# Performance work log

Measured on AMD Instinct MI355X. Metric: run time of the kernel, lower is better.

The kernel has to match this reference:

```python
import jax, jax.numpy as jnp
import numpy as np

R = 16
LORA_ALPHA = 16
SCALING = LORA_ALPHA / R  # 1.0


def setup_inputs() -> dict:
    key = jax.random.key(0)
    kx, kr, ka = jax.random.split(key, 3)
    B, S, D, DO, E = 4, 2048, 4096, 4096, 8
    x = jax.random.normal(kx, (B, S, D), dtype=jnp.float32)
    # kaiming_uniform_(a=sqrt(5)) on Linear weight of fan_in=D -> U(-1/sqrt(D), 1/sqrt(D))
    bound_r = 1.0 / np.sqrt(D)
    route_w = jax.random.uniform(kr, (E, D), jnp.float32, -bound_r, bound_r)  # lora_route.weight
    bound_a = 1.0 / np.sqrt(D)
    A = jax.random.uniform(ka, (E, R, D), jnp.float32, -bound_a, bound_a)  # stacked lora_A{i}.weight [r, D]
    # lora_B weights are zero-initialized in the module; use small random for a nontrivial baseline
    kb = jax.random.fold_in(key, 7)
    Bw = jax.random.normal(kb, (E, DO, R), dtype=jnp.float32) * 0.02  # stacked lora_B{i}.weight [DO, r]
    return {"x": x, "route_w": route_w, "A": A, "Bw": Bw}


def reference(x, route_w, A, Bw):
    # router logits [B, S, E]
    logits = jnp.einsum("bsd,ed->bse", x, route_w)
    # top-1 hard routing: keep raw logit value at the argmax slot, zero elsewhere
    topk_v, topk_idx = jax.lax.top_k(logits, 1)  # [B,S,1]
    E = logits.shape[-1]
    route_weight = jax.nn.one_hot(topk_idx[..., 0], E, dtype=logits.dtype) * topk_v  # [B,S,E]
    # low-rank per-expert projections (dense over experts, as in the original loop)
    h = jnp.einsum("bsd,erd->bser", x, A)            # [B,S,E,r]
    wh = route_weight[..., None] * h                  # weight before the up-projection
    out = jnp.einsum("bser,eor->bso", wh, Bw) * SCALING  # [B,S,DO]
    return out
```

## Files before the change

kernel.cpp:

```cpp
#include <hip/hip_runtime.h>
#include <hip/hip_bf16.h>

#define DD   4096
#define NE   8
#define NR   16
#define NTOK 8192
#define NDO  4096
#define TAU  0.01f
#define MAXFLAG 8000

typedef __attribute__((ext_vector_type(8))) __bf16 bf16x8;
typedef __attribute__((ext_vector_type(4))) __bf16 bf16x4;
typedef __attribute__((ext_vector_type(4))) float  f32x4;

__device__ __forceinline__ bf16x8 to_bf16x8(float4 a, float4 b) {
    bf16x8 r;
    r[0] = (__bf16)a.x; r[1] = (__bf16)a.y; r[2] = (__bf16)a.z; r[3] = (__bf16)a.w;
    r[4] = (__bf16)b.x; r[5] = (__bf16)b.y; r[6] = (__bf16)b.z; r[7] = (__bf16)b.w;
    return r;
}

__device__ __forceinline__ bf16x8 zero_frag() {
    bf16x8 z;
    #pragma unroll
    for (int j = 0; j < 8; j++) z[j] = (__bf16)0.0f;
    return z;
}

__global__ __launch_bounds__(256) void k_prep_w(const float* __restrict__ rw,
                                                const float* __restrict__ Am,
                                                const float* __restrict__ Bw,
                                                __bf16* __restrict__ rwhl,
                                                __bf16* __restrict__ Ab,
                                                __bf16* __restrict__ Bwb) {
    const int b = blockIdx.x;
    if (b < 1024) {
        const int o = (b & 511) * 1024 + threadIdx.x * 4;
        const float4 v = *(const float4*)(((b < 512) ? Bw : Am) + o);
        bf16x4 p;
        p[0] = (__bf16)v.x; p[1] = (__bf16)v.y; p[2] = (__bf16)v.z; p[3] = (__bf16)v.w;
        *(bf16x4*)(((b < 512) ? Bwb : Ab) + o) = p;
    } else {
        const int o = (b - 1024) * 1024 + threadIdx.x * 4;
        const int row = o >> 12, k = o & 4095;
        const float4 v = *(const float4*)(rw + ((size_t)(row & 7) << 12) + k);
        bf16x4 p;
        if (row < 8) {
            p[0] = (__bf16)v.x; p[1] = (__bf16)v.y; p[2] = (__bf16)v.z; p[3] = (__bf16)v.w;
        } else {
            p[0] = (__bf16)(v.x - (float)(__bf16)v.x);
            p[1] = (__bf16)(v.y - (float)(__bf16)v.y);
            p[2] = (__bf16)(v.z - (float)(__bf16)v.z);
            p[3] = (__bf16)(v.w - (float)(__bf16)v.w);
        }
        *(bf16x4*)(rwhl + o) = p;
    }
}

__global__ __launch_bounds__(256, 1) void k_route_part(const float* __restrict__ x,
                                                       const __bf16* __restrict__ rwhl,
                                                       float* __restrict__ pbuf) {
    const int tg = blockIdx.x >> 2;
    const int kg = blockIdx.x & 3;
    const int t0 = tg * 16;
    const int wv = threadIdx.x >> 6;
    const int lane = threadIdx.x & 63;
    const int m = lane & 15;
    const int half = lane >> 4;

    const float*  xrow = x    + (size_t)(t0 + m) * DD;
    const __bf16* wrow = rwhl + (size_t)m * DD;

    f32x4 acc = {0.f, 0.f, 0.f, 0.f};
    const int kbase = kg * 1024 + wv * 256;
    #pragma unroll
    for (int ks = 0; ks < 8; ks++) {
        const int k0 = kbase + ks * 32 + half * 8;
        const float4 xa = *(const float4*)(xrow + k0);
        const float4 xc = *(const float4*)(xrow + k0 + 4);
        const bf16x8 wb = *(const bf16x8*)(wrow + k0);
        acc = __builtin_amdgcn_mfma_f32_16x16x32_bf16(to_bf16x8(xa, xc), wb, acc, 0, 0, 0);
    }

    __shared__ float Lred[4][16][17];
    #pragma unroll
    for (int r = 0; r < 4; r++)
        Lred[wv][half * 4 + r][m] = acc[r];
    __syncthreads();

    if (threadIdx.x < 128) {
        const int t = threadIdx.x >> 3, ee = threadIdx.x & 7;
        float s = 0.f;
        #pragma unroll
        for (int w = 0; w < 4; w++) s += Lred[w][t][ee] + Lred[w][t][ee + 8];
        pbuf[((size_t)kg * NTOK + t0 + t) * NE + ee] = s;
    }
}

__global__ __launch_bounds__(256) void k_route_fin(const float* __restrict__ pbuf,
                                                   float* __restrict__ w_arr,
                                                   int*   __restrict__ token_list,
                                                   int*   __restrict__ count,
                                                   int*   __restrict__ nflag,
                                                   int*   __restrict__ flaglist) {
    const int tok = blockIdx.x * 256 + threadIdx.x;
    float l[NE];
    #pragma unroll
    for (int e = 0; e < NE; e++)
        l[e] = pbuf[((size_t)0 * NTOK + tok) * NE + e]
             + pbuf[((size_t)1 * NTOK + tok) * NE + e]
             + pbuf[((size_t)2 * NTOK + tok) * NE + e]
             + pbuf[((size_t)3 * NTOK + tok) * NE + e];

    float best = -1e30f, second = -1e30f; int be = 0;
    #pragma unroll
    for (int e = 0; e < NE; e++) {
        if (l[e] > best) { second = best; best = l[e]; be = e; }
        else if (l[e] > second) { second = l[e]; }
    }
    w_arr[tok] = best;
    if (best - second < TAU) {
        const int p = atomicAdd(nflag, 1);
        if (p < MAXFLAG) flaglist[p] = tok;
    } else {
        const int p = atomicAdd(&count[be], 1);
        token_list[be * NTOK + p] = tok;
    }
}

__global__ __launch_bounds__(256) void k_fix(const float* __restrict__ x,
                                             const float* __restrict__ rw,
                                             float* __restrict__ w_arr,
                                             int*   __restrict__ token_list,
                                             int*   __restrict__ count,
                                             const int* __restrict__ nflag,
                                             const int* __restrict__ flaglist) {
    const int wv   = threadIdx.x >> 6;
    const int lane = threadIdx.x & 63;
    int n = *nflag; if (n > MAXFLAG) n = MAXFLAG;

    for (int idx = blockIdx.x * 4 + wv; idx < n; idx += 512) {
        const int tok = flaglist[idx];
        const float* xp = x + (size_t)tok * DD;
        double acc[NE];
        #pragma unroll
        for (int e = 0; e < NE; e++) acc[e] = 0.0;
        for (int i = 0; i < 16; i++) {
            const int d4 = (i * 64 + lane) * 4;
            const float4 xv = *(const float4*)(xp + d4);
            const double x0 = xv.x, x1 = xv.y, x2 = xv.z, x3 = xv.w;
            #pragma unroll
            for (int e = 0; e < NE; e++) {
                const float4 wv4 = *(const float4*)(rw + (size_t)e * DD + d4);
                acc[e] = fma(x0, (double)wv4.x, acc[e]);
                acc[e] = fma(x1, (double)wv4.y, acc[e]);
                acc[e] = fma(x2, (double)wv4.z, acc[e]);
                acc[e] = fma(x3, (double)wv4.w, acc[e]);
            }
        }
        #pragma unroll
        for (int off = 32; off > 0; off >>= 1)
            #pragma unroll
            for (int e = 0; e < NE; e++)
                acc[e] += __shfl_xor(acc[e], off, 64);
        if (lane == 0) {
            double best = acc[0]; int be = 0;
            #pragma unroll
            for (int e = 1; e < NE; e++) if (acc[e] > best) { best = acc[e]; be = e; }
            w_arr[tok] = (float)best;
            const int pos = atomicAdd(&count[be], 1);
            token_list[be * NTOK + pos] = tok;
        }
    }
}

__global__ __launch_bounds__(1024) void k_h(const float* __restrict__ x,
                                            const __bf16* __restrict__ Ab,
                                            const float* __restrict__ w_arr,
                                            const int*   __restrict__ token_list,
                                            const int*   __restrict__ count,
                                            __hip_bfloat16* __restrict__ wh) {
    const int e    = blockIdx.x >> 7;
    const int g    = blockIdx.x & 127;
    const int cnt  = count[e];
    const int base = g * 32;
    if (base >= cnt) return;

    const int wv   = threadIdx.x >> 6;
    const int lane = threadIdx.x & 63;
    const int m    = lane & 15;
    const int half = lane >> 4;

    const int i0 = base + m,  i1 = base + 16 + m;
    const int tok0 = (i0 < cnt) ? token_list[e * NTOK + i0] : 0;
    const int tok1 = (i1 < cnt) ? token_list[e * NTOK + i1] : 0;
    const float*  xr0  = x  + (size_t)tok0 * DD;
    const float*  xr1  = x  + (size_t)tok1 * DD;
    const __bf16* arow = Ab + ((size_t)e * NR + m) * DD;

    f32x4 acc0 = {0.f,0.f,0.f,0.f}, acc1 = {0.f,0.f,0.f,0.f};
    const int kbase = wv * 256;
    #pragma unroll
    for (int kc = 0; kc < 8; kc++) {
        const int k0 = kbase + kc * 32 + half * 8;
        const bf16x8 bfrag = *(const bf16x8*)(arow + k0);
        const bf16x8 a0 = to_bf16x8(*(const float4*)(xr0 + k0),
                                    *(const float4*)(xr0 + k0 + 4));
        const bf16x8 a1 = to_bf16x8(*(const float4*)(xr1 + k0),
                                    *(const float4*)(xr1 + k0 + 4));
        acc0 = __builtin_amdgcn_mfma_f32_16x16x32_bf16(a0, bfrag, acc0, 0, 0, 0);
        acc1 = __builtin_amdgcn_mfma_f32_16x16x32_bf16(a1, bfrag, acc1, 0, 0, 0);
    }

    __shared__ float lds[16][32][17];
    #pragma unroll
    for (int rr = 0; rr < 4; rr++) {
        lds[wv][half * 4 + rr][m]      = acc0[rr];
        lds[wv][16 + half * 4 + rr][m] = acc1[rr];
    }
    __syncthreads();

    if (threadIdx.x < 512) {
        const int t = threadIdx.x >> 4;
        const int r = threadIdx.x & 15;
        const int i2 = base + t;
        if (i2 < cnt) {
            float s = 0.f;
            #pragma unroll
            for (int w = 0; w < 16; w++) s += lds[w][t][r];
            const int tk = token_list[e * NTOK + i2];
            wh[(size_t)tk * NR + r] = (__hip_bfloat16)(s * w_arr[tk]);
        }
    }
}

__global__ __launch_bounds__(256) void k_out(const __bf16* __restrict__ Bwb,
                                             const __hip_bfloat16* __restrict__ wh,
                                             const int*   __restrict__ token_list,
                                             const int*   __restrict__ count,
                                             float* __restrict__ out) {
    const int bx    = blockIdx.x;
    const int e     = bx >> 10;
    const int slot  = (bx >> 3) & 127;
    const int chunk = bx & 7;
    const int cnt   = count[e];
    const int base  = slot * 64;
    if (base >= cnt) return;

    const int wv   = threadIdx.x >> 6;
    const int lane = threadIdx.x & 63;
    const int m    = lane & 15;
    const int half = lane >> 4;
    const int h2   = (half < 2) ? half : 0;
    const bf16x8 zf = zero_frag();

    bf16x8 a2[4]; int trow[4]; bool vst[4];
    #pragma unroll
    for (int s = 0; s < 4; s++) {
        const int idx = base + s * 16 + m;
        vst[s]  = idx < cnt;
        trow[s] = vst[s] ? token_list[e * NTOK + idx] : 0;
        a2[s] = (half < 2 && vst[s])
            ? *(const bf16x8*)((const __bf16*)wh + (size_t)trow[s] * NR + half * 8)
            : zf;
    }

    const __bf16* bwe = Bwb + (size_t)e * NDO * NR;
    const int ot0 = chunk * 32 + wv * 8;
    const f32x4 zero4 = {0.f, 0.f, 0.f, 0.f};

    bf16x8 bq = (half < 2)
        ? *(const bf16x8*)(bwe + (size_t)(ot0 * 16 + m) * NR + h2 * 8)
        : zf;
    #pragma unroll
    for (int i = 0; i < 8; i++) {
        const bf16x8 b2 = bq;
        if (i < 7) {
            bq = (half < 2)
                ? *(const bf16x8*)(bwe + (size_t)((ot0 + i + 1) * 16 + m) * NR + h2 * 8)
                : zf;
        }
        const int ob = (ot0 + i) * 16;
        #pragma unroll
        for (int s = 0; s < 4; s++) {
            const f32x4 d = __builtin_amdgcn_mfma_f32_16x16x32_bf16(b2, a2[s], zero4, 0, 0, 0);
            if (vst[s])
                __builtin_nontemporal_store(d,
                    (f32x4*)(out + (size_t)trow[s] * NDO + ob + half * 4));
        }
    }
}

extern "C" void kernel_launch(void* const* d_in, const int* in_sizes, int n_in,
                              void* d_out, int out_size, void* d_ws, size_t ws_size,
                              hipStream_t stream) {
    const float* x  = (const float*)d_in[0];
    const float* rw = (const float*)d_in[1];
    const float* Am = (const float*)d_in[2];
    const float* Bw = (const float*)d_in[3];
    float* out = (float*)d_out;

    char* ws = (char*)d_ws;
    int*   count      = (int*)ws;
    int*   nflag      = (int*)(ws + 32);
    float* w_arr      = (float*)(ws + 512);
    int*   flaglist   = (int*)(ws + 33280);
    int*   token_list = (int*)(ws + 65536);
    __hip_bfloat16* wh = (__hip_bfloat16*)(ws + 327680);
    __bf16* rwhl      = (__bf16*)(ws + 589824);
    __bf16* Bwb       = (__bf16*)(ws + 720896);
    __bf16* Ab        = (__bf16*)(ws + 1769472);
    float*  pbuf      = (float*)(ws + 3145728);

    hipMemsetAsync(ws, 0, 64, stream);
    hipLaunchKernelGGL(k_prep_w,     dim3(1088),  dim3(256), 0, stream, rw, Am, Bw, rwhl, Ab, Bwb);
    hipLaunchKernelGGL(k_route_part, dim3(2048),  dim3(256), 0, stream, x, rwhl, pbuf);
    hipLaunchKernelGGL(k_route_fin,  dim3(32),    dim3(256), 0, stream, pbuf, w_arr, token_list, count, nflag, flaglist);
    hipLaunchKernelGGL(k_fix,        dim3(128),   dim3(256), 0, stream, x, rw, w_arr, token_list, count, nflag, flaglist);
    hipLaunchKernelGGL(k_h,          dim3(1024),  dim3(1024),0, stream, x, Ab, w_arr, token_list, count, wh);
    hipLaunchKernelGGL(k_out,        dim3(8192),  dim3(256), 0, stream, Bwb, wh, token_list, count, out);
}
```

Before: 172.0 us.

## Fuse expert down-projection into router pass and stage output tiles through LDS

The router kernel now also computes the low-rank projections for all 8 experts in the same pass over x, writing K-split partials that the finalize kernel reduces and scales for the chosen expert. This removes the separate gather kernel that re-read x per expert. Flagged near-tie tokens recompute h in the fix kernel. The output kernel now builds 64x128 tiles in shared memory and writes full contiguous rows, rather than scattered 16-byte stores. The cost is 8x more MFMA work and A reads in the router pass, plus a larger partial buffer written and read back.

```diff
diff --git a/kernel.cpp b/kernel.cpp
--- a/kernel.cpp
+++ b/kernel.cpp
@@ -57,9 +57,11 @@
     }
 }
 
-__global__ __launch_bounds__(256, 1) void k_route_part(const float* __restrict__ x,
-                                                       const __bf16* __restrict__ rwhl,
-                                                       float* __restrict__ pbuf) {
+__global__ __launch_bounds__(256, 1) void k_rh(const float* __restrict__ x,
+                                               const __bf16* __restrict__ rwhl,
+                                               const __bf16* __restrict__ Ab,
+                                               float* __restrict__ pbufL,
+                                               float* __restrict__ pbufH) {
     const int tg = blockIdx.x >> 2;
     const int kg = blockIdx.x & 3;
     const int t0 = tg * 16;
@@ -70,22 +72,32 @@
 
     const float*  xrow = x    + (size_t)(t0 + m) * DD;
     const __bf16* wrow = rwhl + (size_t)m * DD;
-
-    f32x4 acc = {0.f, 0.f, 0.f, 0.f};
     const int kbase = kg * 1024 + wv * 256;
+
+    f32x4 accR = {0.f, 0.f, 0.f, 0.f};
+    f32x4 accE[NE];
+    #pragma unroll
+    for (int e = 0; e < NE; e++) accE[e] = (f32x4){0.f, 0.f, 0.f, 0.f};
+
     #pragma unroll
     for (int ks = 0; ks < 8; ks++) {
         const int k0 = kbase + ks * 32 + half * 8;
         const float4 xa = *(const float4*)(xrow + k0);
         const float4 xc = *(const float4*)(xrow + k0 + 4);
         const bf16x8 wb = *(const bf16x8*)(wrow + k0);
-        acc = __builtin_amdgcn_mfma_f32_16x16x32_bf16(to_bf16x8(xa, xc), wb, acc, 0, 0, 0);
+        const bf16x8 xf = to_bf16x8(xa, xc);
+        accR = __builtin_amdgcn_mfma_f32_16x16x32_bf16(xf, wb, accR, 0, 0, 0);
+        #pragma unroll
+        for (int e = 0; e < NE; e++) {
+            const bf16x8 af = *(const bf16x8*)(Ab + ((size_t)e * NR + m) * DD + k0);
+            accE[e] = __builtin_amdgcn_mfma_f32_16x16x32_bf16(xf, af, accE[e], 0, 0, 0);
+        }
     }
 
     __shared__ float Lred[4][16][17];
     #pragma unroll
     for (int r = 0; r < 4; r++)
-        Lred[wv][half * 4 + r][m] = acc[r];
+        Lred[wv][half * 4 + r][m] = accR[r];
     __syncthreads();
 
     if (threadIdx.x < 128) {
@@ -93,24 +105,46 @@
         float s = 0.f;
         #pragma unroll
         for (int w = 0; w < 4; w++) s += Lred[w][t][ee] + Lred[w][t][ee + 8];
-        pbuf[((size_t)kg * NTOK + t0 + t) * NE + ee] = s;
-    }
-}
-
-__global__ __launch_bounds__(256) void k_route_fin(const float* __restrict__ pbuf,
-                                                   float* __restrict__ w_arr,
-                                                   int*   __restrict__ token_list,
-                                                   int*   __restrict__ count,
-                                                   int*   __restrict__ nflag,
-                                                   int*   __restrict__ flaglist) {
+        pbufL[((size_t)kg * NTOK + t0 + t) * NE + ee] = s;
+    }
+
+    __shared__ float hbuf[4][16][2][17];
+    #pragma unroll
+    for (int eg = 0; eg < 4; eg++) {
+        __syncthreads();
+        #pragma unroll
+        for (int r = 0; r < 4; r++) {
+            hbuf[wv][half * 4 + r][0][m] = accE[eg * 2][r];
+            hbuf[wv][half * 4 + r][1][m] = accE[eg * 2 + 1][r];
+        }
+        __syncthreads();
+        #pragma unroll
+        for (int q = 0; q < 2; q++) {
+            const int idx = q * 256 + threadIdx.x;
+            const int t = idx >> 5, e2 = (idx >> 4) & 1, r = idx & 15;
+            const float s = hbuf[0][t][e2][r] + hbuf[1][t][e2][r]
+                          + hbuf[2][t][e2][r] + hbuf[3][t][e2][r];
+            pbufH[(((size_t)kg * NTOK + t0 + t) * NE + eg * 2 + e2) * NR + r] = s;
+        }
+    }
+}
+
+__global__ __launch_bounds__(256) void k_fin(const float* __restrict__ pbufL,
+                                             const float* __restrict__ pbufH,
+                                             float* __restrict__ w_arr,
+                                             __bf16* __restrict__ wh,
+                                             int*   __restrict__ token_list,
+                                             int*   __restrict__ count,
+                                             int*   __restrict__ nflag,
+                                             int*   __restrict__ flaglist) {
     const int tok = blockIdx.x * 256 + threadIdx.x;
     float l[NE];
     #pragma unroll
     for (int e = 0; e < NE; e++)
-        l[e] = pbuf[((size_t)0 * NTOK + tok) * NE + e]
-             + pbuf[((size_t)1 * NTOK + tok) * NE + e]
-             + pbuf[((size_t)2 * NTOK + tok) * NE + e]
-             + pbuf[((size_t)3 * NTOK + tok) * NE + e];
+        l[e] = pbufL[((size_t)0 * NTOK + tok) * NE + e]
+             + pbufL[((size_t)1 * NTOK + tok) * NE + e]
+             + pbufL[((size_t)2 * NTOK + tok) * NE + e]
+             + pbufL[((size_t)3 * NTOK + tok) * NE + e];
 
     float best = -1e30f, second = -1e30f; int be = 0;
     #pragma unroll
@@ -126,11 +160,31 @@
         const int p = atomicAdd(&count[be], 1);
         token_list[be * NTOK + p] = tok;
     }
+
+    float h[NR];
+    #pragma unroll
+    for (int r = 0; r < NR; r++) h[r] = 0.f;
+    #pragma unroll
+    for (int g = 0; g < 4; g++) {
+        #pragma unroll
+        for (int r = 0; r < NR; r++)
+            h[r] += pbufH[(((size_t)g * NTOK + tok) * NE + be) * NR + r];
+    }
+    bf16x8 w0, w1;
+    #pragma unroll
+    for (int r = 0; r < 8; r++) {
+        w0[r] = (__bf16)(h[r] * best);
+        w1[r] = (__bf16)(h[r + 8] * best);
+    }
+    *(bf16x8*)(wh + (size_t)tok * NR)     = w0;
+    *(bf16x8*)(wh + (size_t)tok * NR + 8) = w1;
 }
 
 __global__ __launch_bounds__(256) void k_fix(const float* __restrict__ x,
                                              const float* __restrict__ rw,
+                                             const __bf16* __restrict__ Ab,
                                              float* __restrict__ w_arr,
+                                             __bf16* __restrict__ wh,
                                              int*   __restrict__ token_list,
                                              int*   __restrict__ count,
                                              const int* __restrict__ nflag,
@@ -163,85 +217,48 @@
             #pragma unroll
             for (int e = 0; e < NE; e++)
                 acc[e] += __shfl_xor(acc[e], off, 64);
+
+        double best = acc[0]; int be = 0;
+        #pragma unroll
+        for (int e = 1; e < NE; e++) if (acc[e] > best) { best = acc[e]; be = e; }
+        const float bw = (float)best;
+
+        float h[NR];
+        #pragma unroll
+        for (int r = 0; r < NR; r++) h[r] = 0.f;
+        const __bf16* abase = Ab + (size_t)be * NR * DD;
+        for (int i = 0; i < 64; i++) {
+            const int k = i * 64 + lane;
+            const float xv = xp[k];
+            #pragma unroll
+            for (int r = 0; r < NR; r++)
+                h[r] = fmaf(xv, (float)abase[(size_t)r * DD + k], h[r]);
+        }
+        #pragma unroll
+        for (int off = 32; off > 0; off >>= 1)
+            #pragma unroll
+            for (int r = 0; r < NR; r++)
+                h[r] += __shfl_xor(h[r], off, 64);
+
         if (lane == 0) {
-            double best = acc[0]; int be = 0;
-            #pragma unroll
-            for (int e = 1; e < NE; e++) if (acc[e] > best) { best = acc[e]; be = e; }
-            w_arr[tok] = (float)best;
+            w_arr[tok] = bw;
             const int pos = atomicAdd(&count[be], 1);
             token_list[be * NTOK + pos] = tok;
-        }
-    }
-}
-
-__global__ __launch_bounds__(1024) void k_h(const float* __restrict__ x,
-                                            const __bf16* __restrict__ Ab,
-                                            const float* __restrict__ w_arr,
-                                            const int*   __restrict__ token_list,
-                                            const int*   __restrict__ count,
-                                            __hip_bfloat16* __restrict__ wh) {
-    const int e    = blockIdx.x >> 7;
-    const int g    = blockIdx.x & 127;
-    const int cnt  = count[e];
-    const int base = g * 32;
-    if (base >= cnt) return;
-
-    const int wv   = threadIdx.x >> 6;
-    const int lane = threadIdx.x & 63;
-    const int m    = lane & 15;
-    const int half = lane >> 4;
-
-    const int i0 = base + m,  i1 = base + 16 + m;
-    const int tok0 = (i0 < cnt) ? token_list[e * NTOK + i0] : 0;
-    const int tok1 = (i1 < cnt) ? token_list[e * NTOK + i1] : 0;
-    const float*  xr0  = x  + (size_t)tok0 * DD;
-    const float*  xr1  = x  + (size_t)tok1 * DD;
-    const __bf16* arow = Ab + ((size_t)e * NR + m) * DD;
-
-    f32x4 acc0 = {0.f,0.f,0.f,0.f}, acc1 = {0.f,0.f,0.f,0.f};
-    const int kbase = wv * 256;
-    #pragma unroll
-    for (int kc = 0; kc < 8; kc++) {
-        const int k0 = kbase + kc * 32 + half * 8;
-        const bf16x8 bfrag = *(const bf16x8*)(arow + k0);
-        const bf16x8 a0 = to_bf16x8(*(const float4*)(xr0 + k0),
-                                    *(const float4*)(xr0 + k0 + 4));
-        const bf16x8 a1 = to_bf16x8(*(const float4*)(xr1 + k0),
-                                    *(const float4*)(xr1 + k0 + 4));
-        acc0 = __builtin_amdgcn_mfma_f32_16x16x32_bf16(a0, bfrag, acc0, 0, 0, 0);
-        acc1 = __builtin_amdgcn_mfma_f32_16x16x32_bf16(a1, bfrag, acc1, 0, 0, 0);
-    }
-
-    __shared__ float lds[16][32][17];
-    #pragma unroll
-    for (int rr = 0; rr < 4; rr++) {
-        lds[wv][half * 4 + rr][m]      = acc0[rr];
-        lds[wv][16 + half * 4 + rr][m] = acc1[rr];
-    }
-    __syncthreads();
-
-    if (threadIdx.x < 512) {
-        const int t = threadIdx.x >> 4;
-        const int r = threadIdx.x & 15;
-        const int i2 = base + t;
-        if (i2 < cnt) {
-            float s = 0.f;
-            #pragma unroll
-            for (int w = 0; w < 16; w++) s += lds[w][t][r];
-            const int tk = token_list[e * NTOK + i2];
-            wh[(size_t)tk * NR + r] = (__hip_bfloat16)(s * w_arr[tk]);
-        }
-    }
-}
-
-__global__ __launch_bounds__(256) void k_out(const __bf16* __restrict__ Bwb,
-                                             const __hip_bfloat16* __restrict__ wh,
-                                             const int*   __restrict__ token_list,
-                                             const int*   __restrict__ count,
-                                             float* __restrict__ out) {
+            #pragma unroll
+            for (int r = 0; r < NR; r++)
+                wh[(size_t)tok * NR + r] = (__bf16)(h[r] * bw);
+        }
+    }
+}
+
+__global__ __launch_bounds__(256, 1) void k_out(const __bf16* __restrict__ Bwb,
+                                                const __bf16* __restrict__ wh,
+                                                const int*   __restrict__ token_list,
+                                                const int*   __restrict__ count,
+                                                float* __restrict__ out) {
     const int bx    = blockIdx.x;
-    const int e     = bx >> 10;
-    const int slot  = (bx >> 3) & 127;
+    const int e     = bx >> 9;
+    const int slot  = (bx >> 3) & 63;
     const int chunk = bx & 7;
     const int cnt   = count[e];
     const int base  = slot * 64;
@@ -254,39 +271,45 @@
     const int h2   = (half < 2) ? half : 0;
     const bf16x8 zf = zero_frag();
 
-    bf16x8 a2[4]; int trow[4]; bool vst[4];
+    bf16x8 a2[4];
     #pragma unroll
     for (int s = 0; s < 4; s++) {
         const int idx = base + s * 16 + m;
-        vst[s]  = idx < cnt;
-        trow[s] = vst[s] ? token_list[e * NTOK + idx] : 0;
-        a2[s] = (half < 2 && vst[s])
-            ? *(const bf16x8*)((const __bf16*)wh + (size_t)trow[s] * NR + half * 8)
-            : zf;
-    }
-
+        const bool v  = idx < cnt;
+        const int tk  = v ? token_list[e * NTOK + idx] : 0;
+        a2[s] = (half < 2 && v) ? *(const bf16x8*)(wh + (size_t)tk * NR + half * 8) : zf;
+    }
+
+    __shared__ float tile[64][136];
     const __bf16* bwe = Bwb + (size_t)e * NDO * NR;
-    const int ot0 = chunk * 32 + wv * 8;
     const f32x4 zero4 = {0.f, 0.f, 0.f, 0.f};
 
-    bf16x8 bq = (half < 2)
-        ? *(const bf16x8*)(bwe + (size_t)(ot0 * 16 + m) * NR + h2 * 8)
-        : zf;
-    #pragma unroll
-    for (int i = 0; i < 8; i++) {
-        const bf16x8 b2 = bq;
-        if (i < 7) {
-            bq = (half < 2)
-                ? *(const bf16x8*)(bwe + (size_t)((ot0 + i + 1) * 16 + m) * NR + h2 * 8)
+    for (int hf = 0; hf < 4; hf++) {
+        const int cb = chunk * 512 + hf * 128;
+        if (hf) __syncthreads();
+        #pragma unroll
+        for (int i = 0; i < 2; i++) {
+            const int oc = cb + (wv * 2 + i) * 16;
+            const bf16x8 b2 = (half < 2)
+                ? *(const bf16x8*)(bwe + (size_t)(oc + m) * NR + h2 * 8)
                 : zf;
-        }
-        const int ob = (ot0 + i) * 16;
-        #pragma unroll
-        for (int s = 0; s < 4; s++) {
-            const f32x4 d = __builtin_amdgcn_mfma_f32_16x16x32_bf16(b2, a2[s], zero4, 0, 0, 0);
-            if (vst[s])
-                __builtin_nontemporal_store(d,
-                    (f32x4*)(out + (size_t)trow[s] * NDO + ob + half * 4));
+            #pragma unroll
+            for (int s = 0; s < 4; s++) {
+                const f32x4 d = __builtin_amdgcn_mfma_f32_16x16x32_bf16(b2, a2[s], zero4, 0, 0, 0);
+                *(f32x4*)&tile[s * 16 + m][(wv * 2 + i) * 16 + half * 4] = d;
+            }
+        }
+        __syncthreads();
+        #pragma unroll
+        for (int it = 0; it < 8; it++) {
+            const int r  = it * 8 + (threadIdx.x >> 5);
+            const int ir = base + r;
+            if (ir < cnt) {
+                const int tk = token_list[e * NTOK + ir];
+                const int c  = (threadIdx.x & 31) * 4;
+                const f32x4 v = *(const f32x4*)&tile[r][c];
+                __builtin_nontemporal_store(v, (f32x4*)(out + (size_t)tk * NDO + cb + c));
+            }
         }
     }
 }
@@ -306,17 +329,17 @@
     float* w_arr      = (float*)(ws + 512);
     int*   flaglist   = (int*)(ws + 33280);
     int*   token_list = (int*)(ws + 65536);
-    __hip_bfloat16* wh = (__hip_bfloat16*)(ws + 327680);
+    __bf16* wh        = (__bf16*)(ws + 327680);
     __bf16* rwhl      = (__bf16*)(ws + 589824);
     __bf16* Bwb       = (__bf16*)(ws + 720896);
     __bf16* Ab        = (__bf16*)(ws + 1769472);
-    float*  pbuf      = (float*)(ws + 3145728);
+    float*  pbufL     = (float*)(ws + 3145728);
+    float*  pbufH     = (float*)(ws + 4194304);
 
     hipMemsetAsync(ws, 0, 64, stream);
-    hipLaunchKernelGGL(k_prep_w,     dim3(1088),  dim3(256), 0, stream, rw, Am, Bw, rwhl, Ab, Bwb);
-    hipLaunchKernelGGL(k_route_part, dim3(2048),  dim3(256), 0, stream, x, rwhl, pbuf);
-    hipLaunchKernelGGL(k_route_fin,  dim3(32),    dim3(256), 0, stream, pbuf, w_arr, token_list, count, nflag, flaglist);
-    hipLaunchKernelGGL(k_fix,        dim3(128),   dim3(256), 0, stream, x, rw, w_arr, token_list, count, nflag, flaglist);
-    hipLaunchKernelGGL(k_h,          dim3(1024),  dim3(1024),0, stream, x, Ab, w_arr, token_list, count, wh);
-    hipLaunchKernelGGL(k_out,        dim3(8192),  dim3(256), 0, stream, Bwb, wh, token_list, count, out);
-}
+    hipLaunchKernelGGL(k_prep_w, dim3(1088), dim3(256), 0, stream, rw, Am, Bw, rwhl, Ab, Bwb);
+    hipLaunchKernelGGL(k_rh,     dim3(2048), dim3(256), 0, stream, x, rwhl, Ab, pbufL, pbufH);
+    hipLaunchKernelGGL(k_fin,    dim3(32),   dim3(256), 0, stream, pbufL, pbufH, w_arr, wh, token_list, count, nflag, flaglist);
+    hipLaunchKernelGGL(k_fix,    dim3(128),  dim3(256), 0, stream, x, rw, Ab, w_arr, wh, token_list, count, nflag, flaglist);
+    hipLaunchKernelGGL(k_out,    dim3(4096), dim3(256), 0, stream, Bwb, wh, token_list, count, out);
+}
```

After: 206.1 us. +19.9%, slower.

## Restructure up-projection kernel to token-ordered tiles with LDS-staged coalesced stores

Applied to the files above, without the earlier changes.

The output kernel now walks tokens in natural order instead of per-expert gathered lists. A per-token expert id array is written during routing. Each block handles 64 consecutive tokens and loops over all 8 experts, issuing MFMAs only where a 16-token group contains that expert and masking the other rows. Results are staged through an LDS tile so each block writes contiguous 128-column row segments instead of scattered 16-byte stores. The cost is extra MFMA work and B-weight loads for every expert present in a group, plus LDS traffic and barriers.

```diff
diff --git a/kernel.cpp b/kernel.cpp
--- a/kernel.cpp
+++ b/kernel.cpp
@@ -99,6 +99,7 @@
 
 __global__ __launch_bounds__(256) void k_route_fin(const float* __restrict__ pbuf,
                                                    float* __restrict__ w_arr,
+                                                   int*   __restrict__ eid,
                                                    int*   __restrict__ token_list,
                                                    int*   __restrict__ count,
                                                    int*   __restrict__ nflag,
@@ -119,6 +120,7 @@
         else if (l[e] > second) { second = l[e]; }
     }
     w_arr[tok] = best;
+    eid[tok]   = be;
     if (best - second < TAU) {
         const int p = atomicAdd(nflag, 1);
         if (p < MAXFLAG) flaglist[p] = tok;
@@ -131,6 +133,7 @@
 __global__ __launch_bounds__(256) void k_fix(const float* __restrict__ x,
                                              const float* __restrict__ rw,
                                              float* __restrict__ w_arr,
+                                             int*   __restrict__ eid,
                                              int*   __restrict__ token_list,
                                              int*   __restrict__ count,
                                              const int* __restrict__ nflag,
@@ -168,6 +171,7 @@
             #pragma unroll
             for (int e = 1; e < NE; e++) if (acc[e] > best) { best = acc[e]; be = e; }
             w_arr[tok] = (float)best;
+            eid[tok]   = be;
             const int pos = atomicAdd(&count[be], 1);
             token_list[be * NTOK + pos] = tok;
         }
@@ -179,7 +183,7 @@
                                             const float* __restrict__ w_arr,
                                             const int*   __restrict__ token_list,
                                             const int*   __restrict__ count,
-                                            __hip_bfloat16* __restrict__ wh) {
+                                            __bf16* __restrict__ wh) {
     const int e    = blockIdx.x >> 7;
     const int g    = blockIdx.x & 127;
     const int cnt  = count[e];
@@ -229,24 +233,18 @@
             #pragma unroll
             for (int w = 0; w < 16; w++) s += lds[w][t][r];
             const int tk = token_list[e * NTOK + i2];
-            wh[(size_t)tk * NR + r] = (__hip_bfloat16)(s * w_arr[tk]);
-        }
-    }
-}
-
-__global__ __launch_bounds__(256) void k_out(const __bf16* __restrict__ Bwb,
-                                             const __hip_bfloat16* __restrict__ wh,
-                                             const int*   __restrict__ token_list,
-                                             const int*   __restrict__ count,
-                                             float* __restrict__ out) {
-    const int bx    = blockIdx.x;
-    const int e     = bx >> 10;
-    const int slot  = (bx >> 3) & 127;
-    const int chunk = bx & 7;
-    const int cnt   = count[e];
-    const int base  = slot * 64;
-    if (base >= cnt) return;
-
+            wh[(size_t)tk * NR + r] = (__bf16)(s * w_arr[tk]);
+        }
+    }
+}
+
+__global__ __launch_bounds__(512, 8) void k_out(const __bf16* __restrict__ Bwb,
+                                                const __bf16* __restrict__ wh,
+                                                const int* __restrict__ eid,
+                                                float* __restrict__ out) {
+    const int tg = blockIdx.x >> 3;
+    const int ch = blockIdx.x & 7;
+    const int t0 = tg * 64;
     const int wv   = threadIdx.x >> 6;
     const int lane = threadIdx.x & 63;
     const int m    = lane & 15;
@@ -254,39 +252,51 @@
     const int h2   = (half < 2) ? half : 0;
     const bf16x8 zf = zero_frag();
 
-    bf16x8 a2[4]; int trow[4]; bool vst[4];
+    bf16x8 a2[4]; int es[4];
     #pragma unroll
     for (int s = 0; s < 4; s++) {
-        const int idx = base + s * 16 + m;
-        vst[s]  = idx < cnt;
-        trow[s] = vst[s] ? token_list[e * NTOK + idx] : 0;
-        a2[s] = (half < 2 && vst[s])
-            ? *(const bf16x8*)((const __bf16*)wh + (size_t)trow[s] * NR + half * 8)
-            : zf;
-    }
-
-    const __bf16* bwe = Bwb + (size_t)e * NDO * NR;
-    const int ot0 = chunk * 32 + wv * 8;
+        const int tok = t0 + s * 16 + m;
+        es[s] = eid[tok];
+        a2[s] = (half < 2) ? *(const bf16x8*)(wh + (size_t)tok * NR + half * 8) : zf;
+    }
+
+    __shared__ float tile[64][132];
     const f32x4 zero4 = {0.f, 0.f, 0.f, 0.f};
 
-    bf16x8 bq = (half < 2)
-        ? *(const bf16x8*)(bwe + (size_t)(ot0 * 16 + m) * NR + h2 * 8)
-        : zf;
-    #pragma unroll
-    for (int i = 0; i < 8; i++) {
-        const bf16x8 b2 = bq;
-        if (i < 7) {
-            bq = (half < 2)
-                ? *(const bf16x8*)(bwe + (size_t)((ot0 + i + 1) * 16 + m) * NR + h2 * 8)
+    for (int hf = 0; hf < 4; hf++) {
+        const int cb = ch * 512 + hf * 128;
+        const int oc = cb + wv * 16;
+
+        if (hf) __syncthreads();
+
+        f32x4 acc0 = zero4, acc1 = zero4, acc2 = zero4, acc3 = zero4;
+        #pragma unroll
+        for (int e = 0; e < NE; e++) {
+            const bf16x8 b2 = (half < 2)
+                ? *(const bf16x8*)(Bwb + ((size_t)e * NDO + oc + m) * NR + h2 * 8)
                 : zf;
-        }
-        const int ob = (ot0 + i) * 16;
-        #pragma unroll
-        for (int s = 0; s < 4; s++) {
-            const f32x4 d = __builtin_amdgcn_mfma_f32_16x16x32_bf16(b2, a2[s], zero4, 0, 0, 0);
-            if (vst[s])
-                __builtin_nontemporal_store(d,
-                    (f32x4*)(out + (size_t)trow[s] * NDO + ob + half * 4));
+            if (__ballot(es[0] == e)) acc0 = __builtin_amdgcn_mfma_f32_16x16x32_bf16(es[0] == e ? a2[0] : zf, b2, acc0, 0, 0, 0);
+            if (__ballot(es[1] == e)) acc1 = __builtin_amdgcn_mfma_f32_16x16x32_bf16(es[1] == e ? a2[1] : zf, b2, acc1, 0, 0, 0);
+            if (__ballot(es[2] == e)) acc2 = __builtin_amdgcn_mfma_f32_16x16x32_bf16(es[2] == e ? a2[2] : zf, b2, acc2, 0, 0, 0);
+            if (__ballot(es[3] == e)) acc3 = __builtin_amdgcn_mfma_f32_16x16x32_bf16(es[3] == e ? a2[3] : zf, b2, acc3, 0, 0, 0);
+        }
+        #pragma unroll
+        for (int r = 0; r < 4; r++) {
+            tile[ 0 + half * 4 + r][wv * 16 + m] = acc0[r];
+            tile[16 + half * 4 + r][wv * 16 + m] = acc1[r];
+            tile[32 + half * 4 + r][wv * 16 + m] = acc2[r];
+            tile[48 + half * 4 + r][wv * 16 + m] = acc3[r];
+        }
+        __syncthreads();
+
+        #pragma unroll
+        for (int rnd = 0; rnd < 4; rnd++) {
+            const int idx = rnd * 512 + threadIdx.x;
+            const int row = idx >> 5;
+            const int c4  = idx & 31;
+            const f32x4 v = *(const f32x4*)&tile[row][c4 * 4];
+            __builtin_nontemporal_store(v,
+                (f32x4*)(out + (size_t)(t0 + row) * NDO + cb + c4 * 4));
         }
     }
 }
@@ -306,17 +316,18 @@
     float* w_arr      = (float*)(ws + 512);
     int*   flaglist   = (int*)(ws + 33280);
     int*   token_list = (int*)(ws + 65536);
-    __hip_bfloat16* wh = (__hip_bfloat16*)(ws + 327680);
+    __bf16* wh        = (__bf16*)(ws + 327680);
     __bf16* rwhl      = (__bf16*)(ws + 589824);
     __bf16* Bwb       = (__bf16*)(ws + 720896);
     __bf16* Ab        = (__bf16*)(ws + 1769472);
     float*  pbuf      = (float*)(ws + 3145728);
+    int*    eid       = (int*)(ws + 4194304);
 
     hipMemsetAsync(ws, 0, 64, stream);
-    hipLaunchKernelGGL(k_prep_w,     dim3(1088),  dim3(256), 0, stream, rw, Am, Bw, rwhl, Ab, Bwb);
-    hipLaunchKernelGGL(k_route_part, dim3(2048),  dim3(256), 0, stream, x, rwhl, pbuf);
-    hipLaunchKernelGGL(k_route_fin,  dim3(32),    dim3(256), 0, stream, pbuf, w_arr, token_list, count, nflag, flaglist);
-    hipLaunchKernelGGL(k_fix,        dim3(128),   dim3(256), 0, stream, x, rw, w_arr, token_list, count, nflag, flaglist);
-    hipLaunchKernelGGL(k_h,          dim3(1024),  dim3(1024),0, stream, x, Ab, w_arr, token_list, count, wh);
-    hipLaunchKernelGGL(k_out,        dim3(8192),  dim3(256), 0, stream, Bwb, wh, token_list, count, out);
-}
+    hipLaunchKernelGGL(k_prep_w,     dim3(1088), dim3(256), 0, stream, rw, Am, Bw, rwhl, Ab, Bwb);
+    hipLaunchKernelGGL(k_route_part, dim3(2048), dim3(256), 0, stream, x, rwhl, pbuf);
+    hipLaunchKernelGGL(k_route_fin,  dim3(32),   dim3(256), 0, stream, pbuf, w_arr, eid, token_list, count, nflag, flaglist);
+    hipLaunchKernelGGL(k_fix,        dim3(128),  dim3(256), 0, stream, x, rw, w_arr, eid, token_list, count, nflag, flaglist);
+    hipLaunchKernelGGL(k_h,          dim3(1024), dim3(1024),0, stream, x, Ab, w_arr, token_list, count, wh);
+    hipLaunchKernelGGL(k_out,        dim3(1024), dim3(512), 0, stream, Bwb, wh, eid, out);
+}
```

Result: slower. 367.6 us (+113.8%).
